# Kernel optimization log

Measured on AMD Instinct MI355X. Metric: run time of the kernel, lower is better.

The kernel has to match this reference:

```python
import jax, jax.numpy as jnp
import numpy as np

E = 2048
H = 16
D = E // H  # head_dim = 128
S_SLOTS = 8
EPS = 1e-5


def _linear_params(key, fan_in, fan_out):
    kw, kb = jax.random.split(key)
    lim = 1.0 / np.sqrt(fan_in)
    W = jax.random.uniform(kw, (fan_out, fan_in), jnp.float32, -lim, lim)
    b = jax.random.uniform(kb, (fan_out,), jnp.float32, -lim, lim)
    return W, b


def setup_inputs() -> dict:
    key = jax.random.key(0)
    ks = jax.random.split(key, 10)
    x = jax.random.normal(ks[0], (2, 2048, E), jnp.float32)
    thought_slots = jax.random.normal(ks[1], (S_SLOTS, E), jnp.float32)
    Wq, bq = _linear_params(ks[2], E, E)
    Wk, bk = _linear_params(ks[3], E, E)
    Wv, bv = _linear_params(ks[4], E, E)
    Wtq, btq = _linear_params(ks[5], E, E)
    Wtk, btk = _linear_params(ks[6], E, E)
    Wtv, btv = _linear_params(ks[7], E, E)
    Wo, bo = _linear_params(ks[8], E, E)
    gamma = jnp.ones((E,), jnp.float32)
    beta = jnp.zeros((E,), jnp.float32)
    return dict(x=x, thought_slots=thought_slots, Wq=Wq, bq=bq, Wk=Wk, bk=bk,
                Wv=Wv, bv=bv, Wtq=Wtq, btq=btq, Wtk=Wtk, btk=btk,
                Wtv=Wtv, btv=btv, Wo=Wo, bo=bo, gamma=gamma, beta=beta)


def _heads(t, B):
    # [B, S, E] -> [B, H, S, D]
    return t.reshape(B, -1, H, D).transpose(0, 2, 1, 3)


def reference(x, thought_slots, Wq, bq, Wk, bk, Wv, bv,
              Wtq, btq, Wtk, btk, Wtv, btv, Wo, bo, gamma, beta):
    B, S, _ = x.shape
    scale = 1.0 / np.sqrt(D)

    # regular self-attention stream
    q = _heads(x @ Wq.T + bq, B)
    k = _heads(x @ Wk.T + bk, B)
    v = _heads(x @ Wv.T + bv, B)
    attn = jax.nn.softmax(jnp.einsum('bhqd,bhkd->bhqk', q, k) * scale, axis=-1)
    regular_out = jnp.einsum('bhqk,bhkd->bhqd', attn, v)

    # thought cross-attention stream (keys/values from learned slots)
    slots = jnp.broadcast_to(thought_slots, (B, S_SLOTS, thought_slots.shape[-1]))
    t_q = _heads(x @ Wtq.T + btq, B)
    t_k = _heads(slots @ Wtk.T + btk, B)
    t_v = _heads(slots @ Wtv.T + btv, B)
    t_attn = jax.nn.softmax(jnp.einsum('bhqd,bhkd->bhqk', t_q, t_k) * scale, axis=-1)
    thought_out = jnp.einsum('bhqk,bhkd->bhqd', t_attn, t_v)

    # merge heads, combine, layernorm, output projection
    combined = (regular_out + thought_out).transpose(0, 2, 1, 3).reshape(B, S, E)
    mu = jnp.mean(combined, axis=-1, keepdims=True)
    var = jnp.var(combined, axis=-1, keepdims=True)
    normed = (combined - mu) * jax.lax.rsqrt(var + EPS) * gamma + beta
    return normed @ Wo.T + bo
```

## Files before the change

### kernel.cpp

```cpp
#include <hip/hip_runtime.h>
#include <hip/hip_bf16.h>
#include <stdint.h>

typedef __bf16 bf16;
typedef __bf16 bf16x8 __attribute__((ext_vector_type(8)));
typedef __bf16 bf16x4 __attribute__((ext_vector_type(4)));
typedef float f32x4 __attribute__((ext_vector_type(4)));
typedef float f32x16 __attribute__((ext_vector_type(16)));
typedef uint32_t u32x2 __attribute__((ext_vector_type(2)));
typedef uint32_t u32x4 __attribute__((ext_vector_type(4)));

#define E_DIM 2048
#define HEADS 16
#define HD 128
#define SEQ 2048
#define BATCH 2
#define NTOK 4096
#define NSLOT 8

#define QSCALE (0.08838834764831845f * 1.4426950408889634f)

#define WAITV(N) asm volatile("s_waitcnt vmcnt(" #N ")" ::: "memory")

__device__ __forceinline__ void gload_lds16(const void* g, void* lds) {
  __builtin_amdgcn_global_load_lds(
      (const __attribute__((address_space(1))) uint32_t*)g,
      (__attribute__((address_space(3))) uint32_t*)lds, 16, 0, 0);
}

__global__ __launch_bounds__(256) void cvt_f32_bf16_kernel(
    const float* __restrict__ src, bf16* __restrict__ dst, int n8)
{
  for (int i = blockIdx.x * 256 + threadIdx.x; i < n8; i += gridDim.x * 256) {
    const f32x4 a = *(const f32x4*)(src + i * 8);
    const f32x4 b = *(const f32x4*)(src + i * 8 + 4);
    bf16x8 o;
#pragma unroll
    for (int j = 0; j < 4; j++) { o[j] = (bf16)a[j]; o[4 + j] = (bf16)b[j]; }
    *(bf16x8*)(dst + i * 8) = o;
  }
}

struct CvtArgs { const float* src[5]; bf16* dst[5]; };

__global__ __launch_bounds__(256) void cvt5_kernel(CvtArgs a, int n8)
{
  const float* __restrict__ src = a.src[blockIdx.y];
  bf16* __restrict__ dst = a.dst[blockIdx.y];
  for (int i = blockIdx.x * 256 + threadIdx.x; i < n8; i += gridDim.x * 256) {
    const f32x4 x = *(const f32x4*)(src + i * 8);
    const f32x4 y = *(const f32x4*)(src + i * 8 + 4);
    bf16x8 o;
#pragma unroll
    for (int j = 0; j < 4; j++) { o[j] = (bf16)x[j]; o[4 + j] = (bf16)y[j]; }
    *(bf16x8*)(dst + i * 8) = o;
  }
}

struct ProjArgs {
  const bf16* W[4];
  const float* bias[4];
  void* out[4];
  int mode[4];
  float scale[4];
};

__global__ __launch_bounds__(512, 2) void gemm256_kernel(
    const bf16* __restrict__ A, ProjArgs pa, int nbm, int nbn)
{
  __shared__ char As_[2 * 32768];
  __shared__ char Bs_[2 * 32768];

  const int nwg = gridDim.x;
  const int qch = nwg >> 3;
  const int wg = (blockIdx.x & 7) * qch + (blockIdx.x >> 3);
  const int bm = wg % nbm;
  const int rest = wg / nbm;
  const int bn = rest % nbn;
  const int z = rest / nbn;

  const bf16* __restrict__ W = pa.W[z];
  const float* __restrict__ bias = pa.bias[z];
  void* __restrict__ out = pa.out[z];
  const int mode = pa.mode[z];
  const float scale = pa.scale[z];

  const int tid = threadIdx.x;
  const int lane = tid & 63;
  const int w = tid >> 6;
  const int wr = w >> 2;
  const int wc = w & 3;
  const int g = lane >> 4, c = lane & 15;

  const int srow = tid >> 3;
  const int sslot = tid & 7;
  const int scol = (sslot ^ (srow & 7)) * 8;
  const bf16* Abase = A + (size_t)(bm * 256) * 2048;
  const bf16* Bbase = W + (size_t)(bn * 256) * 2048;

  auto stageB = [&](int T, int u) {
    char* dst = Bs_ + (T & 1) * 32768 + u * 16384;
    const int k0 = T * 64;
#pragma unroll
    for (int j = 0; j < 2; j++) {
      const int r = u * 128 + srow + j * 64;
      gload_lds16(Bbase + (size_t)r * 2048 + k0 + scol,
                  dst + (size_t)(srow + j * 64) * 128 + sslot * 16);
    }
  };
  auto stageA = [&](int T, int u) {
    char* dst = As_ + (T & 1) * 32768 + u * 16384;
    const int k0 = T * 64;
#pragma unroll
    for (int j = 0; j < 2; j++) {
      const int r = j * 128 + u * 64 + srow;
      gload_lds16(Abase + (size_t)r * 2048 + k0 + scol,
                  dst + (size_t)(srow + j * 64) * 128 + sslot * 16);
    }
  };

  f32x4 acc[8][4] = {};
  bf16x8 bfr[4][2];

  stageB(0, 0); stageB(0, 1); stageA(0, 0); stageA(0, 1);
  stageB(1, 0); stageB(1, 1); stageA(1, 0);
  WAITV(6);
  __builtin_amdgcn_s_barrier();

  const int NT = 2048 / 64;
  for (int t = 0; t < NT; t++) {
    const int d = t & 1;
    const char* Aq = As_ + d * 32768;
    const char* Bq = Bs_ + d * 32768;
#pragma unroll
    for (int q = 0; q < 4; q++) {
      bf16x8 af[2][2];
      if (q == 0) {
#pragma unroll
        for (int n = 0; n < 4; n++)
#pragma unroll
          for (int kk = 0; kk < 2; kk++) {
            const int row = wc * 64 + n * 16 + c;
            bfr[n][kk] = *(const bf16x8*)(Bq + (size_t)row * 128 +
                                          (((kk * 4 + g) ^ (c & 7)) * 16));
          }
      }
#pragma unroll
      for (int mi2 = 0; mi2 < 2; mi2++)
#pragma unroll
        for (int kk = 0; kk < 2; kk++) {
          const int row = wr * 128 + (q * 2 + mi2) * 16 + c;
          const int slab = (row >> 6) & 1;
          const int aoff = (row & 63) + ((row >> 7) << 6);
          af[mi2][kk] = *(const bf16x8*)(Aq + slab * 16384 + (size_t)aoff * 128 +
                                         (((kk * 4 + g) ^ (c & 7)) * 16));
        }

      if (q == 0)      { if (t + 1 < NT) stageA(t + 1, 1); }
      else if (q == 2) { if (t + 2 < NT) stageB(t + 2, 0); }
      else if (q == 3) { if (t + 2 < NT) { stageB(t + 2, 1); stageA(t + 2, 0); } }

      __builtin_amdgcn_s_setprio(1);
#pragma unroll
      for (int mi2 = 0; mi2 < 2; mi2++)
#pragma unroll
        for (int n = 0; n < 4; n++)
#pragma unroll
          for (int kk = 0; kk < 2; kk++)
            acc[q * 2 + mi2][n] = __builtin_amdgcn_mfma_f32_16x16x32_bf16(
                af[mi2][kk], bfr[n][kk], acc[q * 2 + mi2][n], 0, 0, 0);
      __builtin_amdgcn_s_setprio(0);

      if (q == 1) {
        __builtin_amdgcn_s_barrier();
      } else if (q == 3) {
        if (t < NT - 2)       { WAITV(6); }
        else if (t == NT - 2) { WAITV(0); }
        __builtin_amdgcn_s_barrier();
      }
    }
  }

#pragma unroll
  for (int mi = 0; mi < 8; mi++) {
#pragma unroll
    for (int n = 0; n < 4; n++) {
      const int col = bn * 256 + wc * 64 + n * 16 + c;
      const float bv = bias[col];
#pragma unroll
      for (int j = 0; j < 4; j++) {
        const int row = bm * 256 + wr * 128 + mi * 16 + g * 4 + j;
        const float v = (acc[mi][n][j] + bv) * scale;
        const int b = row >> 11, s = row & 2047;
        const int h = col >> 7, d2 = col & 127;
        size_t idx;
        if (mode == 1) idx = (((size_t)(b * HEADS + h)) * SEQ + s) * HD + d2;
        else           idx = (((size_t)(b * HEADS + h)) * HD + d2) * SEQ + s;
        ((bf16*)out)[idx] = (bf16)v;
      }
    }
  }
}

__global__ __launch_bounds__(512, 2) void gemm256k_kernel(
    const bf16* __restrict__ A, const bf16* __restrict__ W,
    bf16* __restrict__ P0, bf16* __restrict__ P1)
{
  __shared__ char As_[2 * 32768];
  __shared__ char Bs_[2 * 32768];

  const int nwg = gridDim.x;
  const int qch = nwg >> 3;
  const int wg = (blockIdx.x & 7) * qch + (blockIdx.x >> 3);
  const int bm = wg % 16;
  const int rest = wg / 16;
  const int bn = rest & 7;
  const int ks = rest >> 3;
  bf16* __restrict__ out = ks ? P1 : P0;
  const int kbase = ks * 1024;

  const int tid = threadIdx.x;
  const int lane = tid & 63;
  const int w = tid >> 6;
  const int wr = w >> 2;
  const int wc = w & 3;
  const int g = lane >> 4, c = lane & 15;

  const int srow = tid >> 3;
  const int sslot = tid & 7;
  const int scol = (sslot ^ (srow & 7)) * 8;
  const bf16* Abase = A + (size_t)(bm * 256) * 2048;
  const bf16* Bbase = W + (size_t)(bn * 256) * 2048;

  auto stageB = [&](int T, int u) {
    char* dst = Bs_ + (T & 1) * 32768 + u * 16384;
    const int k0 = kbase + T * 64;
#pragma unroll
    for (int j = 0; j < 2; j++) {
      const int r = u * 128 + srow + j * 64;
      gload_lds16(Bbase + (size_t)r * 2048 + k0 + scol,
                  dst + (size_t)(srow + j * 64) * 128 + sslot * 16);
    }
  };
  auto stageA = [&](int T, int u) {
    char* dst = As_ + (T & 1) * 32768 + u * 16384;
    const int k0 = kbase + T * 64;
#pragma unroll
    for (int j = 0; j < 2; j++) {
      const int r = j * 128 + u * 64 + srow;
      gload_lds16(Abase + (size_t)r * 2048 + k0 + scol,
                  dst + (size_t)(srow + j * 64) * 128 + sslot * 16);
    }
  };

  f32x4 acc[8][4] = {};
  bf16x8 bfr[4][2];

  stageB(0, 0); stageB(0, 1); stageA(0, 0); stageA(0, 1);
  stageB(1, 0); stageB(1, 1); stageA(1, 0);
  WAITV(6);
  __builtin_amdgcn_s_barrier();

  const int NT = 16;
  for (int t = 0; t < NT; t++) {
    const int d = t & 1;
    const char* Aq = As_ + d * 32768;
    const char* Bq = Bs_ + d * 32768;
#pragma unroll
    for (int q = 0; q < 4; q++) {
      bf16x8 af[2][2];
      if (q == 0) {
#pragma unroll
        for (int n = 0; n < 4; n++)
#pragma unroll
          for (int kk = 0; kk < 2; kk++) {
            const int row = wc * 64 + n * 16 + c;
            bfr[n][kk] = *(const bf16x8*)(Bq + (size_t)row * 128 +
                                          (((kk * 4 + g) ^ (c & 7)) * 16));
          }
      }
#pragma unroll
      for (int mi2 = 0; mi2 < 2; mi2++)
#pragma unroll
        for (int kk = 0; kk < 2; kk++) {
          const int row = wr * 128 + (q * 2 + mi2) * 16 + c;
          const int slab = (row >> 6) & 1;
          const int aoff = (row & 63) + ((row >> 7) << 6);
          af[mi2][kk] = *(const bf16x8*)(Aq + slab * 16384 + (size_t)aoff * 128 +
                                         (((kk * 4 + g) ^ (c & 7)) * 16));
        }

      if (q == 0)      { if (t + 1 < NT) stageA(t + 1, 1); }
      else if (q == 2) { if (t + 2 < NT) stageB(t + 2, 0); }
      else if (q == 3) { if (t + 2 < NT) { stageB(t + 2, 1); stageA(t + 2, 0); } }

      __builtin_amdgcn_s_setprio(1);
#pragma unroll
      for (int mi2 = 0; mi2 < 2; mi2++)
#pragma unroll
        for (int n = 0; n < 4; n++)
#pragma unroll
          for (int kk = 0; kk < 2; kk++)
            acc[q * 2 + mi2][n] = __builtin_amdgcn_mfma_f32_16x16x32_bf16(
                af[mi2][kk], bfr[n][kk], acc[q * 2 + mi2][n], 0, 0, 0);
      __builtin_amdgcn_s_setprio(0);

      if (q == 1) {
        __builtin_amdgcn_s_barrier();
      } else if (q == 3) {
        if (t < NT - 2)       { WAITV(6); }
        else if (t == NT - 2) { WAITV(0); }
        __builtin_amdgcn_s_barrier();
      }
    }
  }

#pragma unroll
  for (int mi = 0; mi < 8; mi++) {
#pragma unroll
    for (int n = 0; n < 4; n++) {
      const int col = bn * 256 + wc * 64 + n * 16 + c;
#pragma unroll
      for (int j = 0; j < 4; j++) {
        const int row = bm * 256 + wr * 128 + mi * 16 + g * 4 + j;
        out[(size_t)row * E_DIM + col] = (bf16)acc[mi][n][j];
      }
    }
  }
}

__global__ __launch_bounds__(256) void reduce_bias_kernel(
    const bf16* __restrict__ P0, const bf16* __restrict__ P1,
    const float* __restrict__ bias, float* __restrict__ out, int n8)
{
  for (int i = blockIdx.x * 256 + threadIdx.x; i < n8; i += gridDim.x * 256) {
    const bf16x8 a = *(const bf16x8*)(P0 + (size_t)i * 8);
    const bf16x8 b = *(const bf16x8*)(P1 + (size_t)i * 8);
    const int col = (i * 8) & 2047;
    const f32x4 b0 = *(const f32x4*)(bias + col);
    const f32x4 b1 = *(const f32x4*)(bias + col + 4);
    f32x4 o0, o1;
#pragma unroll
    for (int j = 0; j < 4; j++) {
      o0[j] = (float)a[j] + (float)b[j] + b0[j];
      o1[j] = (float)a[4 + j] + (float)b[4 + j] + b1[j];
    }
    *(f32x4*)(out + (size_t)i * 8) = o0;
    *(f32x4*)(out + (size_t)i * 8 + 4) = o1;
  }
}

__global__ __launch_bounds__(256) void slots_proj_kernel(
    const float* __restrict__ slots,
    const float* __restrict__ Wk, const float* __restrict__ bk,
    const float* __restrict__ Wv, const float* __restrict__ bv,
    float* __restrict__ tk, float* __restrict__ tv)
{
  const int col = blockIdx.x * 256 + threadIdx.x;
  const int slot = blockIdx.y;
  const int mat = blockIdx.z;
  const float* W = mat ? Wv : Wk;
  const float* bias = mat ? bv : bk;
  float* out = mat ? tv : tk;
  const float* xr = slots + (size_t)slot * E_DIM;
  const float* wr = W + (size_t)col * E_DIM;
  float acc = 0.f;
  for (int k = 0; k < E_DIM; k += 4) {
    const f32x4 a = *(const f32x4*)(xr + k);
    const f32x4 b4 = *(const f32x4*)(wr + k);
#pragma unroll
    for (int i = 0; i < 4; i++) acc += a[i] * b4[i];
  }
  out[(size_t)slot * E_DIM + col] = acc + bias[col];
}

__global__ __launch_bounds__(512) void flash_attn_kernel(
    const bf16* __restrict__ Qg, const bf16* __restrict__ Kg,
    const bf16* __restrict__ Vtg, bf16* __restrict__ Og)
{
  __shared__ char Ks[4][64 * 256];
  __shared__ char Vs[4][128 * 128];

  const int orig = blockIdx.x;
  const int logical = (orig & 7) * 32 + (orig >> 3);
  const int qt = logical & 7;
  const int bh = logical >> 3;

  const int tid = threadIdx.x;
  const int lane = tid & 63;
  const int w = tid >> 6;
  const int q = lane & 31;
  const int hi = lane >> 5;
  const int b = bh >> 4, h = bh & 15;
  const int q0 = qt * 256 + w * 32;

  const bf16* Qb = Qg + ((size_t)bh * SEQ + q0) * HD;
  const bf16* Kb = Kg + (size_t)bh * SEQ * HD;
  const bf16* Vb = Vtg + (size_t)bh * HD * SEQ;

  auto stage = [&](int kv0, int buf) {
#pragma unroll
    for (int i = 0; i < 2; i++) {
      const int p = (tid + i * 512) * 16;
      { const int r = p >> 8; const int s16 = (p >> 4) & 15;
        gload_lds16(Kb + (size_t)(kv0 + r) * HD + (s16 ^ (r & 15)) * 8, &Ks[0][0] + buf * 16384 + p); }
      { const int r = p >> 7; const int s8 = (p >> 4) & 7;
        gload_lds16(Vb + (size_t)r * SEQ + kv0 + (s8 ^ (r & 7)) * 8, &Vs[0][0] + buf * 16384 + p); }
    }
  };

  bf16x8 qf[8];
#pragma unroll
  for (int kc = 0; kc < 8; kc++)
    qf[kc] = *(const bf16x8*)(Qb + (size_t)q * HD + kc * 16 + hi * 8);

  f32x16 o[4] = {};
  float mrun = -1e30f, lsum = 0.f;
  bf16x8 pbo[2][2];

  stage(0, 0);
  stage(64, 1);
  WAITV(4);
  __builtin_amdgcn_s_barrier();

  const int NT = SEQ / 64;

  for (int t = 0; t < NT; t++) {
    const int cur = t & 3;
    if (t + 2 < NT) stage((t + 2) * 64, (t + 2) & 3);

    f32x16 st[2] = {};
    const char* Kc = &Ks[0][0] + cur * 16384;
    __builtin_amdgcn_s_setprio(1);
#pragma unroll
    for (int kc = 0; kc < 8; kc++) {
#pragma unroll
      for (int blk = 0; blk < 2; blk++) {
        const int rt = blk * 32 + q;
        const int sl = (2 * kc + hi) ^ (rt & 15);
        const bf16x8 kf = *(const bf16x8*)(Kc + rt * 256 + sl * 16);
        st[blk] = __builtin_amdgcn_mfma_f32_32x32x16_bf16(kf, qf[kc], st[blk], 0, 0, 0);
      }
    }
    __builtin_amdgcn_s_setprio(0);

    float tm[16];
#pragma unroll
    for (int i = 0; i < 16; i++) tm[i] = fmaxf(st[0][i], st[1][i]);
#pragma unroll
    for (int s2 = 8; s2 > 0; s2 >>= 1)
#pragma unroll
      for (int i = 0; i < 8; i++) if (i < s2) tm[i] = fmaxf(tm[i], tm[i + s2]);
    float lm = tm[0];
    lm = fmaxf(lm, __shfl_xor(lm, 32));
    float fsc = 1.0f;
    const bool resc = __any(lm > mrun + 8.0f);
    if (resc) {
      const float mn = fmaxf(mrun, lm);
      fsc = exp2f(mrun - mn);
      mrun = mn;
    }

    float ps0 = 0.f, ps1 = 0.f, ps2 = 0.f, ps3 = 0.f;
#pragma unroll
    for (int blk = 0; blk < 2; blk++)
#pragma unroll
      for (int i = 0; i < 16; i += 4) {
        const float p0 = exp2f(st[blk][i]     - mrun);
        const float p1 = exp2f(st[blk][i + 1] - mrun);
        const float p2 = exp2f(st[blk][i + 2] - mrun);
        const float p3 = exp2f(st[blk][i + 3] - mrun);
        st[blk][i] = p0; st[blk][i + 1] = p1; st[blk][i + 2] = p2; st[blk][i + 3] = p3;
        ps0 += p0; ps1 += p1; ps2 += p2; ps3 += p3;
      }
    lsum = lsum * fsc + ((ps0 + ps1) + (ps2 + ps3));

    bf16x8 pbn[2][2];
#pragma unroll
    for (int blk = 0; blk < 2; blk++)
#pragma unroll
      for (int c2 = 0; c2 < 2; c2++) {
        bf16x4 Lv, Hv;
#pragma unroll
        for (int i = 0; i < 4; i++) {
          Lv[i] = (bf16)st[blk][8 * c2 + i];
          Hv[i] = (bf16)st[blk][8 * c2 + 4 + i];
        }
        const u32x2 Lu = __builtin_bit_cast(u32x2, Lv);
        const u32x2 Hu = __builtin_bit_cast(u32x2, Hv);
        const uint32_t s0 = hi ? Lu.x : Hu.x;
        const uint32_t s1 = hi ? Lu.y : Hu.y;
        const uint32_t x0 = (uint32_t)__shfl_xor((int)s0, 32);
        const uint32_t x1 = (uint32_t)__shfl_xor((int)s1, 32);
        u32x4 bv;
        bv.x = hi ? x0 : Lu.x;
        bv.y = hi ? x1 : Lu.y;
        bv.z = hi ? Hu.x : x0;
        bv.w = hi ? Hu.y : x1;
        pbn[blk][c2] = __builtin_bit_cast(bf16x8, bv);
      }

    if (t > 0) {
      const char* Vc = &Vs[0][0] + ((t - 1) & 3) * 16384;
#pragma unroll
      for (int db = 0; db < 4; db++) {
        const int rt = db * 32 + q;
#pragma unroll
        for (int blk = 0; blk < 2; blk++)
#pragma unroll
          for (int c2 = 0; c2 < 2; c2++) {
            const int sl = (blk * 4 + c2 * 2 + hi) ^ (rt & 7);
            const bf16x8 vf = *(const bf16x8*)(Vc + rt * 128 + sl * 16);
            o[db] = __builtin_amdgcn_mfma_f32_32x32x16_bf16(vf, pbo[blk][c2], o[db], 0, 0, 0);
          }
      }
    }

    if (resc) {
#pragma unroll
      for (int db = 0; db < 4; db++)
#pragma unroll
        for (int i = 0; i < 16; i++) o[db][i] *= fsc;
    }

#pragma unroll
    for (int blk = 0; blk < 2; blk++)
#pragma unroll
      for (int c2 = 0; c2 < 2; c2++) pbo[blk][c2] = pbn[blk][c2];

    if (t < NT - 2)       { WAITV(4); }
    else if (t == NT - 2) { WAITV(0); }
    __builtin_amdgcn_s_barrier();
  }

  {
    const char* Vc = &Vs[0][0] + ((NT - 1) & 3) * 16384;
#pragma unroll
    for (int db = 0; db < 4; db++) {
      const int rt = db * 32 + q;
#pragma unroll
      for (int blk = 0; blk < 2; blk++)
#pragma unroll
        for (int c2 = 0; c2 < 2; c2++) {
          const int sl = (blk * 4 + c2 * 2 + hi) ^ (rt & 7);
          const bf16x8 vf = *(const bf16x8*)(Vc + rt * 128 + sl * 16);
          o[db] = __builtin_amdgcn_mfma_f32_32x32x16_bf16(vf, pbo[blk][c2], o[db], 0, 0, 0);
        }
    }
  }

  const float lt = lsum + __shfl_xor(lsum, 32);
  const float linv = 1.0f / lt;
  bf16* Orow = Og + ((size_t)b * SEQ + q0 + q) * E_DIM + h * HD;
#pragma unroll
  for (int db = 0; db < 4; db++)
#pragma unroll
    for (int g4 = 0; g4 < 4; g4++) {
      bf16x4 ov;
#pragma unroll
      for (int i = 0; i < 4; i++) ov[i] = (bf16)(o[db][g4 * 4 + i] * linv);
      *(bf16x4*)(Orow + db * 32 + g4 * 8 + hi * 4) = ov;
    }
}

__global__ __launch_bounds__(256) void thought_ln_kernel(
    const bf16* __restrict__ TQ, const float* __restrict__ TK,
    const float* __restrict__ TV, const bf16* __restrict__ ATT,
    const float* __restrict__ gamma, const float* __restrict__ beta,
    bf16* __restrict__ Y)
{
  __shared__ float wsum[4], wsq[4];
  const int tid = threadIdx.x;
  const int lane = tid & 63;
  const int w = tid >> 6;
  const int tok = blockIdx.x;
  const int b = tok >> 11, s = tok & 2047;
  const int e0 = tid * 8;
  const int h = e0 >> 7;
  const int d0 = e0 & 127;

  const bf16x8 av = *(const bf16x8*)(ATT + (size_t)tok * E_DIM + e0);
  float v[8];
#pragma unroll
  for (int i = 0; i < 8; i++) v[i] = (float)av[i];

  const bf16x8 qv8 = *(const bf16x8*)(TQ + (((size_t)(b * HEADS + h)) * SEQ + s) * HD + d0);
  float qv[8];
#pragma unroll
  for (int i = 0; i < 8; i++) qv[i] = (float)qv8[i];

  float dts[NSLOT];
#pragma unroll
  for (int sl = 0; sl < NSLOT; sl++) {
    const float* tkr = TK + (size_t)sl * E_DIM + e0;
    const f32x4 k0 = *(const f32x4*)(tkr);
    const f32x4 k1 = *(const f32x4*)(tkr + 4);
    float dp = 0.f;
#pragma unroll
    for (int i = 0; i < 4; i++) dp += qv[i] * k0[i] + qv[4 + i] * k1[i];
    dp += __shfl_xor(dp, 1);
    dp += __shfl_xor(dp, 2);
    dp += __shfl_xor(dp, 4);
    dp += __shfl_xor(dp, 8);
    dts[sl] = dp;
  }
  float mx = dts[0];
#pragma unroll
  for (int sl = 1; sl < NSLOT; sl++) mx = fmaxf(mx, dts[sl]);
  float p[NSLOT], den = 0.f;
#pragma unroll
  for (int sl = 0; sl < NSLOT; sl++) { p[sl] = exp2f(dts[sl] - mx); den += p[sl]; }
  const float dinv = 1.0f / den;
#pragma unroll
  for (int sl = 0; sl < NSLOT; sl++) {
    const float pn = p[sl] * dinv;
    const float* tvr = TV + (size_t)sl * E_DIM + e0;
    const f32x4 v0 = *(const f32x4*)(tvr);
    const f32x4 v1 = *(const f32x4*)(tvr + 4);
#pragma unroll
    for (int i = 0; i < 4; i++) { v[i] += pn * v0[i]; v[4 + i] += pn * v1[i]; }
  }

  float sm = 0.f, sq = 0.f;
#pragma unroll
  for (int i = 0; i < 8; i++) { sm += v[i]; sq += v[i] * v[i]; }
#pragma unroll
  for (int d = 1; d < 64; d <<= 1) { sm += __shfl_xor(sm, d); sq += __shfl_xor(sq, d); }
  if (lane == 0) { wsum[w] = sm; wsq[w] = sq; }
  __syncthreads();
  const float ts = wsum[0] + wsum[1] + wsum[2] + wsum[3];
  const float tq2 = wsq[0] + wsq[1] + wsq[2] + wsq[3];
  const float mean = ts * (1.f / E_DIM);
  const float var = tq2 * (1.f / E_DIM) - mean * mean;
  const float rstd = rsqrtf(var + 1e-5f);
  const f32x4 g0 = *(const f32x4*)(gamma + e0);
  const f32x4 g1 = *(const f32x4*)(gamma + e0 + 4);
  const f32x4 b0 = *(const f32x4*)(beta + e0);
  const f32x4 b1 = *(const f32x4*)(beta + e0 + 4);
  bf16x8 outv;
#pragma unroll
  for (int i = 0; i < 4; i++) {
    outv[i]     = (bf16)((v[i]     - mean) * rstd * g0[i] + b0[i]);
    outv[4 + i] = (bf16)((v[4 + i] - mean) * rstd * g1[i] + b1[i]);
  }
  *(bf16x8*)(Y + (size_t)tok * E_DIM + e0) = outv;
}

extern "C" void kernel_launch(void* const* d_in, const int* in_sizes, int n_in,
                              void* d_out, int out_size, void* d_ws, size_t ws_size,
                              hipStream_t stream) {
  (void)in_sizes; (void)n_in; (void)out_size; (void)ws_size;
  const float* x     = (const float*)d_in[0];
  const float* slots = (const float*)d_in[1];
  const float* Wq  = (const float*)d_in[2];   const float* bq  = (const float*)d_in[3];
  const float* Wk  = (const float*)d_in[4];   const float* bk  = (const float*)d_in[5];
  const float* Wv  = (const float*)d_in[6];   const float* bv  = (const float*)d_in[7];
  const float* Wtq = (const float*)d_in[8];   const float* btq = (const float*)d_in[9];
  const float* Wtk = (const float*)d_in[10];  const float* btk = (const float*)d_in[11];
  const float* Wtv = (const float*)d_in[12];  const float* btv = (const float*)d_in[13];
  const float* Wo  = (const float*)d_in[14];  const float* bo  = (const float*)d_in[15];
  const float* gamma = (const float*)d_in[16];
  const float* beta  = (const float*)d_in[17];

  uint8_t* ws = (uint8_t*)d_ws;
  const size_t BUF  = (size_t)NTOK * E_DIM * sizeof(bf16);
  const size_t WBUF = (size_t)E_DIM * E_DIM * sizeof(bf16);
  bf16* xb   = (bf16*)(ws + 0 * BUF);
  bf16* qb   = (bf16*)(ws + 1 * BUF);
  bf16* kb   = (bf16*)(ws + 2 * BUF);
  bf16* vtb  = (bf16*)(ws + 3 * BUF);
  bf16* tqb  = (bf16*)(ws + 4 * BUF);
  bf16* attb = (bf16*)(ws + 5 * BUF);
  bf16* nrmb = qb;
  bf16* P0   = kb;
  bf16* P1   = vtb;
  uint8_t* wp = ws + 6 * BUF;
  bf16* Wqb  = (bf16*)(wp + 0 * WBUF);
  bf16* Wkb  = (bf16*)(wp + 1 * WBUF);
  bf16* Wvb  = (bf16*)(wp + 2 * WBUF);
  bf16* Wtqb = (bf16*)(wp + 3 * WBUF);
  bf16* Wob  = (bf16*)(wp + 4 * WBUF);
  float* tkb = (float*)(wp + 5 * WBUF);
  float* tvb = (float*)(wp + 5 * WBUF + 128 * 1024);

  const int WN8 = E_DIM * E_DIM / 8;
  const int XN8 = NTOK * E_DIM / 8;
  cvt_f32_bf16_kernel<<<dim3(2048), 256, 0, stream>>>(x, xb, XN8);
  CvtArgs ca;
  ca.src[0] = Wq;  ca.dst[0] = Wqb;
  ca.src[1] = Wk;  ca.dst[1] = Wkb;
  ca.src[2] = Wv;  ca.dst[2] = Wvb;
  ca.src[3] = Wtq; ca.dst[3] = Wtqb;
  ca.src[4] = Wo;  ca.dst[4] = Wob;
  cvt5_kernel<<<dim3(1024, 5), 256, 0, stream>>>(ca, WN8);

  ProjArgs pa;
  pa.W[0] = Wqb;  pa.bias[0] = bq;  pa.out[0] = qb;  pa.mode[0] = 1; pa.scale[0] = QSCALE;
  pa.W[1] = Wkb;  pa.bias[1] = bk;  pa.out[1] = kb;  pa.mode[1] = 1; pa.scale[1] = 1.0f;
  pa.W[2] = Wvb;  pa.bias[2] = bv;  pa.out[2] = vtb; pa.mode[2] = 2; pa.scale[2] = 1.0f;
  pa.W[3] = Wtqb; pa.bias[3] = btq; pa.out[3] = tqb; pa.mode[3] = 1; pa.scale[3] = QSCALE;
  gemm256_kernel<<<dim3(16 * 8 * 4), 512, 0, stream>>>(xb, pa, 16, 8);

  slots_proj_kernel<<<dim3(E_DIM / 256, NSLOT, 2), 256, 0, stream>>>(
      slots, Wtk, btk, Wtv, btv, tkb, tvb);

  flash_attn_kernel<<<dim3((SEQ / 256) * BATCH * HEADS), 512, 0, stream>>>(
      qb, kb, vtb, attb);
  thought_ln_kernel<<<dim3(NTOK), 256, 0, stream>>>(
      tqb, tkb, tvb, attb, gamma, beta, nrmb);

  gemm256k_kernel<<<dim3(256), 512, 0, stream>>>(nrmb, Wob, P0, P1);
  reduce_bias_kernel<<<dim3(2048), 256, 0, stream>>>(
      P0, P1, bo, (float*)d_out, NTOK * E_DIM / 8);
}
```

Before: 423.5 us.

## Simplify projection GEMM to K=32 double-buffered tiles with fewer LDS bytes

Replaces the 256x256 GEMM's K=64 staged pipeline, which split loads into quarter-phases with fine-grained vmcnt waits, with a plain K=32 double buffer and one __syncthreads per iteration. LDS use drops from 128KB to 64KB, and the launch bound now asks for 4 blocks of 512 threads per CU. The aim is higher occupancy and simpler code. In exchange there are twice as many iterations and barriers, the careful overlap of loads with MFMA work is gone, and 4 waves-per-EU likely forces register spilling given the 128 accumulator floats per thread.

```diff
diff --git a/kernel.cpp b/kernel.cpp
--- a/kernel.cpp
+++ b/kernel.cpp
@@ -65,11 +65,11 @@
   float scale[4];
 };
 
-__global__ __launch_bounds__(512, 2) void gemm256_kernel(
+__global__ __launch_bounds__(512, 4) void gemm256_kernel(
     const bf16* __restrict__ A, ProjArgs pa, int nbm, int nbn)
 {
-  __shared__ char As_[2 * 32768];
-  __shared__ char Bs_[2 * 32768];
+  __shared__ bf16 As[2][256 * 32];
+  __shared__ bf16 Bs[2][256 * 32];
 
   const int nwg = gridDim.x;
   const int qch = nwg >> 3;
@@ -92,93 +92,54 @@
   const int wc = w & 3;
   const int g = lane >> 4, c = lane & 15;
 
-  const int srow = tid >> 3;
-  const int sslot = tid & 7;
-  const int scol = (sslot ^ (srow & 7)) * 8;
-  const bf16* Abase = A + (size_t)(bm * 256) * 2048;
-  const bf16* Bbase = W + (size_t)(bn * 256) * 2048;
-
-  auto stageB = [&](int T, int u) {
-    char* dst = Bs_ + (T & 1) * 32768 + u * 16384;
-    const int k0 = T * 64;
+  const int rw = tid >> 2;
+  const int sc = (((tid & 3) ^ ((rw >> 1) & 3))) * 8;
+  const bf16* Asrc = A + (size_t)(bm * 256 + rw) * 2048 + sc;
+  const bf16* Bsrc = W + (size_t)(bn * 256 + rw) * 2048 + sc;
+
+  auto stage = [&](int t, int buf) {
+    const int k0 = t * 32;
 #pragma unroll
     for (int j = 0; j < 2; j++) {
-      const int r = u * 128 + srow + j * 64;
-      gload_lds16(Bbase + (size_t)r * 2048 + k0 + scol,
-                  dst + (size_t)(srow + j * 64) * 128 + sslot * 16);
+      gload_lds16(Asrc + (size_t)(j * 128) * 2048 + k0,
+                  (char*)(&As[buf][0]) + (rw + j * 128) * 64 + (tid & 3) * 16);
+      gload_lds16(Bsrc + (size_t)(j * 128) * 2048 + k0,
+                  (char*)(&Bs[buf][0]) + (rw + j * 128) * 64 + (tid & 3) * 16);
     }
   };
-  auto stageA = [&](int T, int u) {
-    char* dst = As_ + (T & 1) * 32768 + u * 16384;
-    const int k0 = T * 64;
-#pragma unroll
-    for (int j = 0; j < 2; j++) {
-      const int r = j * 128 + u * 64 + srow;
-      gload_lds16(Abase + (size_t)r * 2048 + k0 + scol,
-                  dst + (size_t)(srow + j * 64) * 128 + sslot * 16);
-    }
-  };
 
   f32x4 acc[8][4] = {};
-  bf16x8 bfr[4][2];
-
-  stageB(0, 0); stageB(0, 1); stageA(0, 0); stageA(0, 1);
-  stageB(1, 0); stageB(1, 1); stageA(1, 0);
-  WAITV(6);
-  __builtin_amdgcn_s_barrier();
-
-  const int NT = 2048 / 64;
+  const int fsw = (c >> 1) & 3;
+
+  stage(0, 0);
+  __syncthreads();
+  int cur = 0;
+
+  const int NT = 2048 / 32;
   for (int t = 0; t < NT; t++) {
-    const int d = t & 1;
-    const char* Aq = As_ + d * 32768;
-    const char* Bq = Bs_ + d * 32768;
-#pragma unroll
-    for (int q = 0; q < 4; q++) {
-      bf16x8 af[2][2];
-      if (q == 0) {
-#pragma unroll
-        for (int n = 0; n < 4; n++)
-#pragma unroll
-          for (int kk = 0; kk < 2; kk++) {
-            const int row = wc * 64 + n * 16 + c;
-            bfr[n][kk] = *(const bf16x8*)(Bq + (size_t)row * 128 +
-                                          (((kk * 4 + g) ^ (c & 7)) * 16));
-          }
-      }
-#pragma unroll
-      for (int mi2 = 0; mi2 < 2; mi2++)
-#pragma unroll
-        for (int kk = 0; kk < 2; kk++) {
-          const int row = wr * 128 + (q * 2 + mi2) * 16 + c;
-          const int slab = (row >> 6) & 1;
-          const int aoff = (row & 63) + ((row >> 7) << 6);
-          af[mi2][kk] = *(const bf16x8*)(Aq + slab * 16384 + (size_t)aoff * 128 +
-                                         (((kk * 4 + g) ^ (c & 7)) * 16));
-        }
-
-      if (q == 0)      { if (t + 1 < NT) stageA(t + 1, 1); }
-      else if (q == 2) { if (t + 2 < NT) stageB(t + 2, 0); }
-      else if (q == 3) { if (t + 2 < NT) { stageB(t + 2, 1); stageA(t + 2, 0); } }
-
-      __builtin_amdgcn_s_setprio(1);
-#pragma unroll
-      for (int mi2 = 0; mi2 < 2; mi2++)
-#pragma unroll
-        for (int n = 0; n < 4; n++)
-#pragma unroll
-          for (int kk = 0; kk < 2; kk++)
-            acc[q * 2 + mi2][n] = __builtin_amdgcn_mfma_f32_16x16x32_bf16(
-                af[mi2][kk], bfr[n][kk], acc[q * 2 + mi2][n], 0, 0, 0);
-      __builtin_amdgcn_s_setprio(0);
-
-      if (q == 1) {
-        __builtin_amdgcn_s_barrier();
-      } else if (q == 3) {
-        if (t < NT - 2)       { WAITV(6); }
-        else if (t == NT - 2) { WAITV(0); }
-        __builtin_amdgcn_s_barrier();
-      }
-    }
+    if (t + 1 < NT) stage(t + 1, cur ^ 1);
+
+    bf16x8 af[8], bfr[4];
+#pragma unroll
+    for (int n = 0; n < 4; n++) {
+      const int row = wc * 64 + n * 16 + c;
+      bfr[n] = *(const bf16x8*)((const char*)(&Bs[cur][0]) + row * 64 + ((g ^ fsw) * 16));
+    }
+#pragma unroll
+    for (int mi = 0; mi < 8; mi++) {
+      const int row = wr * 128 + mi * 16 + c;
+      af[mi] = *(const bf16x8*)((const char*)(&As[cur][0]) + row * 64 + ((g ^ fsw) * 16));
+    }
+    __builtin_amdgcn_s_setprio(1);
+#pragma unroll
+    for (int mi = 0; mi < 8; mi++)
+#pragma unroll
+      for (int n = 0; n < 4; n++)
+        acc[mi][n] = __builtin_amdgcn_mfma_f32_16x16x32_bf16(af[mi], bfr[n], acc[mi][n], 0, 0, 0);
+    __builtin_amdgcn_s_setprio(0);
+
+    __syncthreads();
+    cur ^= 1;
   }
 
 #pragma unroll
```

Result: slower. 1.403 ms (+231.2%).
